# Optimization experiments

Measured on AMD Instinct MI355X. Metric: run time of the kernel, lower is better.

Reference implementation:

```python
import jax, jax.numpy as jnp
import numpy as np

KH = KW = 3  # kernel size for both convs


def conv2d_valid(x, w, b):
    # x: [B,C,H,W], w: [O,C,KH,KW], VALID padding, stride 1 (matches nn.Conv2d(3,18,3))
    y = jax.lax.conv_general_dilated(x, w, window_strides=(1, 1), padding='VALID',
                                     dimension_numbers=('NCHW', 'OIHW', 'NCHW'))
    return y + b[None, :, None, None]


def deform_conv2d(x, offset, w, b):
    # Faithful torchvision deform_conv2d: stride 1, pad 0, dilation 1, 1 group, 1 offset group.
    B, C, H, W = x.shape
    O = w.shape[0]
    Ho, Wo = offset.shape[2], offset.shape[3]
    K = KH * KW
    # offset layout: [B, 2*K, Ho, Wo], per-tap (dy, dx) interleaved, taps row-major
    off = offset.reshape(B, K, 2, Ho, Wo)
    dy, dx = off[:, :, 0], off[:, :, 1]                      # [B,K,Ho,Wo]
    ky = jnp.repeat(jnp.arange(KH), KW).astype(x.dtype)       # [K] tap row
    kx = jnp.tile(jnp.arange(KW), KH).astype(x.dtype)         # [K] tap col
    py = dy + jnp.arange(Ho, dtype=x.dtype)[None, None, :, None] + ky[None, :, None, None]
    px = dx + jnp.arange(Wo, dtype=x.dtype)[None, None, None, :] + kx[None, :, None, None]

    y0 = jnp.floor(py); x0 = jnp.floor(px)
    wy = py - y0; wx = px - x0                                # bilinear fractions
    y0i = y0.astype(jnp.int32); x0i = x0.astype(jnp.int32)

    x_flat = x.reshape(B, C, H * W)

    def corner(yi, xi):
        valid = ((yi >= 0) & (yi < H) & (xi >= 0) & (xi < W)).astype(x.dtype)  # zero pad outside
        idx = jnp.clip(yi, 0, H - 1) * W + jnp.clip(xi, 0, W - 1)              # [B,K,Ho,Wo]
        g = jax.vmap(lambda xf, ix: xf[:, ix])(x_flat, idx)                    # [B,C,K,Ho,Wo]
        return g * valid[:, None]

    val = (corner(y0i, x0i)         * ((1 - wy) * (1 - wx))[:, None]
         + corner(y0i, x0i + 1)     * ((1 - wy) * wx)[:, None]
         + corner(y0i + 1, x0i)     * (wy * (1 - wx))[:, None]
         + corner(y0i + 1, x0i + 1) * (wy * wx)[:, None])     # [B,C,K,Ho,Wo]

    out = jnp.einsum('bckhw,ock->bohw', val, w.reshape(O, C, K))
    return out + b[None, :, None, None]


def setup_inputs() -> dict:
    key = jax.random.key(0)
    k1, k2, k3, k4, k5 = jax.random.split(key, 5)
    B, C, H, W = 16, 3, 384, 384
    x = jax.random.normal(k1, (B, C, H, W), dtype=jnp.float32)
    # offset conv: Conv2d(3, 18, 3); scale down so learned offsets stay moderate
    conv_w = jax.random.normal(k2, (18, 3, KH, KW), dtype=jnp.float32) * 0.05
    conv_b = jax.random.normal(k3, (18,), dtype=jnp.float32) * 0.05
    # deform conv: DeformConv2d(3, 3, 3)
    dcn_w = jax.random.normal(k4, (3, 3, KH, KW), dtype=jnp.float32) * (1.0 / np.sqrt(3 * KH * KW))
    dcn_b = jax.random.normal(k5, (3,), dtype=jnp.float32) * 0.05
    return {'x': x, 'conv_w': conv_w, 'conv_b': conv_b, 'dcn_w': dcn_w, 'dcn_b': dcn_b}


def reference(x, conv_w, conv_b, dcn_w, dcn_b):
    offset = conv2d_valid(x, conv_w, conv_b)   # [B,18,H-2,W-2]
    return deform_conv2d(x, offset, dcn_w, dcn_b)  # [B,3,H-2,W-2]
```

## Files before the change

### kernel.cpp

```cpp
#include <hip/hip_runtime.h>

#define BATCH 16
#define CIN   3
#define H     384
#define W     384
#define HW    (H * W)
#define HO    382
#define WO    382
#define OFFC  18
#define OOUT  3
#define KTAPS 9

struct F3 { float a, b, c; };

__global__ __launch_bounds__(256)
void chw_to_hwc_kernel(const float* __restrict__ x, float* __restrict__ xt)
{
    const int gid = blockIdx.x * 256 + threadIdx.x;
    if (gid >= BATCH * HW) return;
    const int b = gid / HW;
    const int p = gid - b * HW;
    const float* xb = x + (size_t)b * (CIN * HW);
    F3 v;
    v.a = xb[p];
    v.b = xb[HW + p];
    v.c = xb[2 * HW + p];
    *(F3*)(xt + (size_t)gid * 3) = v;
}

__global__ __launch_bounds__(256)
void deform_hwc_kernel(const float* __restrict__ xt,
                       const float* __restrict__ conv_w,
                       const float* __restrict__ conv_b,
                       const float* __restrict__ dcn_w,
                       const float* __restrict__ dcn_b,
                       float* __restrict__ out)
{
    const int total = BATCH * HO * WO;
    const int gid = blockIdx.x * 256 + threadIdx.x;
    if (gid >= total) return;

    const int wo  = gid % WO;
    const int tmp = gid / WO;
    const int ho  = tmp % HO;
    const int b   = tmp / HO;

    const float* xtb = xt + (size_t)b * (HW * 3);

    F3 xp[3][3];
    #pragma unroll
    for (int i = 0; i < 3; ++i)
        #pragma unroll
        for (int j = 0; j < 3; ++j)
            xp[i][j] = *(const F3*)(xtb + (size_t)((ho + i) * W + (wo + j)) * 3);

    float off[OFFC];
    #pragma unroll
    for (int o = 0; o < OFFC; ++o) {
        float a = conv_b[o];
        #pragma unroll
        for (int i = 0; i < 3; ++i)
            #pragma unroll
            for (int j = 0; j < 3; ++j) {
                a = fmaf(conv_w[o * 27 + 0 * 9 + i * 3 + j], xp[i][j].a, a);
                a = fmaf(conv_w[o * 27 + 1 * 9 + i * 3 + j], xp[i][j].b, a);
                a = fmaf(conv_w[o * 27 + 2 * 9 + i * 3 + j], xp[i][j].c, a);
            }
        off[o] = a;
    }

    float acc0 = dcn_b[0];
    float acc1 = dcn_b[1];
    float acc2 = dcn_b[2];

    #pragma unroll
    for (int k = 0; k < KTAPS; ++k) {
        const int ky = k / 3;
        const int kx = k % 3;
        const float py = off[2 * k]     + (float)(ho + ky);
        const float px = off[2 * k + 1] + (float)(wo + kx);
        const float y0f = floorf(py);
        const float x0f = floorf(px);
        const float wy = py - y0f;
        const float wx = px - x0f;
        const int y0 = (int)y0f;
        const int x0 = (int)x0f;
        const int y1 = y0 + 1;
        const int x1 = x0 + 1;

        const bool vy0 = (unsigned)y0 < (unsigned)H;
        const bool vy1 = (unsigned)y1 < (unsigned)H;
        const bool vx0 = (unsigned)x0 < (unsigned)W;
        const bool vx1 = (unsigned)x1 < (unsigned)W;

        const int cy0 = min(max(y0, 0), H - 1);
        const int cy1 = min(max(y1, 0), H - 1);
        const int cx0 = min(max(x0, 0), W - 1);
        const int cx1 = min(max(x1, 0), W - 1);

        const float w00 = (vy0 && vx0) ? (1.f - wy) * (1.f - wx) : 0.f;
        const float w01 = (vy0 && vx1) ? (1.f - wy) * wx         : 0.f;
        const float w10 = (vy1 && vx0) ? wy * (1.f - wx)         : 0.f;
        const float w11 = (vy1 && vx1) ? wy * wx                 : 0.f;

        const F3 v00 = *(const F3*)(xtb + (size_t)(cy0 * W + cx0) * 3);
        const F3 v01 = *(const F3*)(xtb + (size_t)(cy0 * W + cx1) * 3);
        const F3 v10 = *(const F3*)(xtb + (size_t)(cy1 * W + cx0) * 3);
        const F3 v11 = *(const F3*)(xtb + (size_t)(cy1 * W + cx1) * 3);

        float s0 = v00.a * w00; s0 = fmaf(v01.a, w01, s0); s0 = fmaf(v10.a, w10, s0); s0 = fmaf(v11.a, w11, s0);
        float s1 = v00.b * w00; s1 = fmaf(v01.b, w01, s1); s1 = fmaf(v10.b, w10, s1); s1 = fmaf(v11.b, w11, s1);
        float s2 = v00.c * w00; s2 = fmaf(v01.c, w01, s2); s2 = fmaf(v10.c, w10, s2); s2 = fmaf(v11.c, w11, s2);

        acc0 = fmaf(dcn_w[0 * 27 + 0 * 9 + k], s0, acc0);
        acc0 = fmaf(dcn_w[0 * 27 + 1 * 9 + k], s1, acc0);
        acc0 = fmaf(dcn_w[0 * 27 + 2 * 9 + k], s2, acc0);
        acc1 = fmaf(dcn_w[1 * 27 + 0 * 9 + k], s0, acc1);
        acc1 = fmaf(dcn_w[1 * 27 + 1 * 9 + k], s1, acc1);
        acc1 = fmaf(dcn_w[1 * 27 + 2 * 9 + k], s2, acc1);
        acc2 = fmaf(dcn_w[2 * 27 + 0 * 9 + k], s0, acc2);
        acc2 = fmaf(dcn_w[2 * 27 + 1 * 9 + k], s1, acc2);
        acc2 = fmaf(dcn_w[2 * 27 + 2 * 9 + k], s2, acc2);
    }

    const int obase = b * (OOUT * HO * WO) + ho * WO + wo;
    __builtin_nontemporal_store(acc0, out + obase);
    __builtin_nontemporal_store(acc1, out + obase + HO * WO);
    __builtin_nontemporal_store(acc2, out + obase + 2 * HO * WO);
}

__global__ __launch_bounds__(256)
void deform_fused_kernel(const float* __restrict__ x,
                         const float* __restrict__ conv_w,
                         const float* __restrict__ conv_b,
                         const float* __restrict__ dcn_w,
                         const float* __restrict__ dcn_b,
                         float* __restrict__ out)
{
    __shared__ float s_cw[OFFC * 27];
    __shared__ float s_cb[OFFC];
    __shared__ float s_dw[OOUT * 27];
    __shared__ float s_db[OOUT];

    const int t = threadIdx.x;
    for (int i = t; i < OFFC * 27; i += 256) s_cw[i] = conv_w[i];
    if (t < OFFC)      s_cb[t] = conv_b[t];
    if (t < OOUT * 27) s_dw[t] = dcn_w[t];
    if (t < OOUT)      s_db[t] = dcn_b[t];
    __syncthreads();

    const int total = BATCH * HO * WO;
    const int gid = blockIdx.x * 256 + t;
    if (gid >= total) return;

    const int wo  = gid % WO;
    const int tmp = gid / WO;
    const int ho  = tmp % HO;
    const int b   = tmp / HO;

    const float* xb = x + b * (CIN * HW);

    float xp[CIN][3][3];
    #pragma unroll
    for (int c = 0; c < CIN; ++c) {
        const float* xc = xb + c * HW + ho * W + wo;
        #pragma unroll
        for (int i = 0; i < 3; ++i)
            #pragma unroll
            for (int j = 0; j < 3; ++j)
                xp[c][i][j] = xc[i * W + j];
    }

    float off[OFFC];
    #pragma unroll
    for (int o = 0; o < OFFC; ++o) {
        float a = s_cb[o];
        const float* wv = &s_cw[o * 27];
        #pragma unroll
        for (int c = 0; c < CIN; ++c)
            #pragma unroll
            for (int i = 0; i < 3; ++i)
                #pragma unroll
                for (int j = 0; j < 3; ++j)
                    a = fmaf(wv[c * 9 + i * 3 + j], xp[c][i][j], a);
        off[o] = a;
    }

    float a0 = s_db[0], a1 = s_db[1], a2 = s_db[2];

    #pragma unroll
    for (int k = 0; k < KTAPS; ++k) {
        const int ky = k / 3;
        const int kx = k % 3;
        const float py = off[2 * k]     + (float)(ho + ky);
        const float px = off[2 * k + 1] + (float)(wo + kx);
        const float y0f = floorf(py);
        const float x0f = floorf(px);
        const float wy = py - y0f;
        const float wx = px - x0f;
        const int y0 = (int)y0f;
        const int x0 = (int)x0f;
        const int y1 = y0 + 1;
        const int x1 = x0 + 1;
        const bool vy0 = (unsigned)y0 < (unsigned)H;
        const bool vy1 = (unsigned)y1 < (unsigned)H;
        const bool vx0 = (unsigned)x0 < (unsigned)W;
        const bool vx1 = (unsigned)x1 < (unsigned)W;
        const int cy0 = min(max(y0, 0), H - 1);
        const int cy1 = min(max(y1, 0), H - 1);
        const int cx0 = min(max(x0, 0), W - 1);
        const int cx1 = min(max(x1, 0), W - 1);
        const float w00 = (vy0 && vx0) ? (1.f - wy) * (1.f - wx) : 0.f;
        const float w01 = (vy0 && vx1) ? (1.f - wy) * wx         : 0.f;
        const float w10 = (vy1 && vx0) ? wy * (1.f - wx)         : 0.f;
        const float w11 = (vy1 && vx1) ? wy * wx                 : 0.f;
        const int i00 = cy0 * W + cx0;
        const int i01 = cy0 * W + cx1;
        const int i10 = cy1 * W + cx0;
        const int i11 = cy1 * W + cx1;
        #pragma unroll
        for (int c = 0; c < CIN; ++c) {
            const float* xc = xb + c * HW;
            float s = xc[i00] * w00;
            s = fmaf(xc[i01], w01, s);
            s = fmaf(xc[i10], w10, s);
            s = fmaf(xc[i11], w11, s);
            a0 = fmaf(s_dw[0 * 27 + c * 9 + k], s, a0);
            a1 = fmaf(s_dw[1 * 27 + c * 9 + k], s, a1);
            a2 = fmaf(s_dw[2 * 27 + c * 9 + k], s, a2);
        }
    }

    const int obase = b * (OOUT * HO * WO) + ho * WO + wo;
    __builtin_nontemporal_store(a0, out + obase);
    __builtin_nontemporal_store(a1, out + obase + HO * WO);
    __builtin_nontemporal_store(a2, out + obase + 2 * HO * WO);
}

extern "C" void kernel_launch(void* const* d_in, const int* in_sizes, int n_in,
                              void* d_out, int out_size, void* d_ws, size_t ws_size,
                              hipStream_t stream) {
    const float* x      = (const float*)d_in[0];
    const float* conv_w = (const float*)d_in[1];
    const float* conv_b = (const float*)d_in[2];
    const float* dcn_w  = (const float*)d_in[3];
    const float* dcn_b  = (const float*)d_in[4];
    float* out = (float*)d_out;

    const int total = BATCH * HO * WO;
    const size_t need = (size_t)BATCH * HW * 3 * sizeof(float);

    if (ws_size >= need) {
        float* xt = (float*)d_ws;
        chw_to_hwc_kernel<<<(BATCH * HW + 255) / 256, 256, 0, stream>>>(x, xt);
        deform_hwc_kernel<<<(total + 255) / 256, 256, 0, stream>>>(
            xt, conv_w, conv_b, dcn_w, dcn_b, out);
    } else {
        deform_fused_kernel<<<(total + 255) / 256, 256, 0, stream>>>(
            x, conv_w, conv_b, dcn_w, dcn_b, out);
    }
}
```

Measured before the change: 161.1 us.

## Use zero-padded float4 HWC staging to drop bounds checks in deform gather

Input staging now writes a float4-per-pixel HWC copy with a two-pixel zero border, so each bilinear corner fetch is one aligned 16-byte load instead of a 12-byte struct load. The new deform kernel clamps into the padded image and no longer computes per-corner validity masks, relying on the zero border for out-of-range samples. This costs a larger staging buffer and more write traffic. Offsets that push a sample more than two pixels outside the image would clamp to a border pixel instead of reading zero. The older path is kept as a fallback when the workspace is too small.

After: 156.1 us. 1.03x faster.

```diff
diff --git a/kernel.cpp b/kernel.cpp
--- a/kernel.cpp
+++ b/kernel.cpp
@@ -11,7 +11,131 @@
 #define OOUT  3
 #define KTAPS 9
 
+#define PAD   2
+#define HP    (H + 2 * PAD)
+#define WP    (W + 2 * PAD)
+
 struct F3 { float a, b, c; };
+
+__global__ __launch_bounds__(256)
+void chw_to_hwc4_kernel(const float* __restrict__ x, float4* __restrict__ xt)
+{
+    const int gid = blockIdx.x * 256 + threadIdx.x;
+    if (gid >= BATCH * HP * WP) return;
+    const int b  = gid / (HP * WP);
+    const int r2 = gid - b * (HP * WP);
+    const int ry = r2 / WP;
+    const int rx = r2 - ry * WP;
+    const int yi = ry - PAD;
+    const int xi = rx - PAD;
+    float4 v = make_float4(0.f, 0.f, 0.f, 0.f);
+    if ((unsigned)yi < (unsigned)H && (unsigned)xi < (unsigned)W) {
+        const float* xb = x + (size_t)b * (CIN * HW);
+        const int p = yi * W + xi;
+        v.x = xb[p];
+        v.y = xb[HW + p];
+        v.z = xb[2 * HW + p];
+    }
+    xt[gid] = v;
+}
+
+__global__ __launch_bounds__(256)
+void deform_pad4_kernel(const float4* __restrict__ xt,
+                        const float* __restrict__ conv_w,
+                        const float* __restrict__ conv_b,
+                        const float* __restrict__ dcn_w,
+                        const float* __restrict__ dcn_b,
+                        float* __restrict__ out)
+{
+    const int total = BATCH * HO * WO;
+    const int gid = blockIdx.x * 256 + threadIdx.x;
+    if (gid >= total) return;
+
+    const int wo  = gid % WO;
+    const int tmp = gid / WO;
+    const int ho  = tmp % HO;
+    const int b   = tmp / HO;
+
+    const float4* xtb = xt + (size_t)b * (HP * WP);
+
+    float4 xp[3][3];
+    #pragma unroll
+    for (int i = 0; i < 3; ++i) {
+        const float4* row = xtb + (ho + i + PAD) * WP + (wo + PAD);
+        xp[i][0] = row[0];
+        xp[i][1] = row[1];
+        xp[i][2] = row[2];
+    }
+
+    float off[OFFC];
+    #pragma unroll
+    for (int o = 0; o < OFFC; ++o) {
+        float a = conv_b[o];
+        #pragma unroll
+        for (int i = 0; i < 3; ++i)
+            #pragma unroll
+            for (int j = 0; j < 3; ++j) {
+                a = fmaf(conv_w[o * 27 + 0 * 9 + i * 3 + j], xp[i][j].x, a);
+                a = fmaf(conv_w[o * 27 + 1 * 9 + i * 3 + j], xp[i][j].y, a);
+                a = fmaf(conv_w[o * 27 + 2 * 9 + i * 3 + j], xp[i][j].z, a);
+            }
+        off[o] = a;
+    }
+
+    float acc0 = dcn_b[0];
+    float acc1 = dcn_b[1];
+    float acc2 = dcn_b[2];
+
+    #pragma unroll
+    for (int k = 0; k < KTAPS; ++k) {
+        const int ky = k / 3;
+        const int kx = k % 3;
+        const float oy = off[2 * k];
+        const float ox = off[2 * k + 1];
+        const float fy = floorf(oy);
+        const float fx = floorf(ox);
+        const float wy = oy - fy;
+        const float wx = ox - fx;
+
+        int iy = (int)fy + (ho + ky + PAD);
+        int ix = (int)fx + (wo + kx + PAD);
+        iy = min(max(iy, 0), HP - 2);
+        ix = min(max(ix, 0), WP - 2);
+
+        const float4* r0 = xtb + iy * WP + ix;
+        const float4* r1 = r0 + WP;
+        const float4 v00 = r0[0];
+        const float4 v01 = r0[1];
+        const float4 v10 = r1[0];
+        const float4 v11 = r1[1];
+
+        const float cwy = 1.f - wy;
+        const float cwx = 1.f - wx;
+        const float w00 = cwy * cwx;
+        const float w01 = cwy * wx;
+        const float w10 = wy * cwx;
+        const float w11 = wy * wx;
+
+        float s0 = v00.x * w00; s0 = fmaf(v01.x, w01, s0); s0 = fmaf(v10.x, w10, s0); s0 = fmaf(v11.x, w11, s0);
+        float s1 = v00.y * w00; s1 = fmaf(v01.y, w01, s1); s1 = fmaf(v10.y, w10, s1); s1 = fmaf(v11.y, w11, s1);
+        float s2 = v00.z * w00; s2 = fmaf(v01.z, w01, s2); s2 = fmaf(v10.z, w10, s2); s2 = fmaf(v11.z, w11, s2);
+
+        acc0 = fmaf(dcn_w[0 * 27 + 0 * 9 + k], s0, acc0);
+        acc0 = fmaf(dcn_w[0 * 27 + 1 * 9 + k], s1, acc0);
+        acc0 = fmaf(dcn_w[0 * 27 + 2 * 9 + k], s2, acc0);
+        acc1 = fmaf(dcn_w[1 * 27 + 0 * 9 + k], s0, acc1);
+        acc1 = fmaf(dcn_w[1 * 27 + 1 * 9 + k], s1, acc1);
+        acc1 = fmaf(dcn_w[1 * 27 + 2 * 9 + k], s2, acc1);
+        acc2 = fmaf(dcn_w[2 * 27 + 0 * 9 + k], s0, acc2);
+        acc2 = fmaf(dcn_w[2 * 27 + 1 * 9 + k], s1, acc2);
+        acc2 = fmaf(dcn_w[2 * 27 + 2 * 9 + k], s2, acc2);
+    }
+
+    const int obase = b * (OOUT * HO * WO) + ho * WO + wo;
+    __builtin_nontemporal_store(acc0, out + obase);
+    __builtin_nontemporal_store(acc1, out + obase + HO * WO);
+    __builtin_nontemporal_store(acc2, out + obase + 2 * HO * WO);
+}
 
 __global__ __launch_bounds__(256)
 void chw_to_hwc_kernel(const float* __restrict__ x, float* __restrict__ xt)
@@ -87,17 +211,14 @@
         const int x0 = (int)x0f;
         const int y1 = y0 + 1;
         const int x1 = x0 + 1;
-
         const bool vy0 = (unsigned)y0 < (unsigned)H;
         const bool vy1 = (unsigned)y1 < (unsigned)H;
         const bool vx0 = (unsigned)x0 < (unsigned)W;
         const bool vx1 = (unsigned)x1 < (unsigned)W;
-
         const int cy0 = min(max(y0, 0), H - 1);
         const int cy1 = min(max(y1, 0), H - 1);
         const int cx0 = min(max(x0, 0), W - 1);
         const int cx1 = min(max(x1, 0), W - 1);
-
         const float w00 = (vy0 && vx0) ? (1.f - wy) * (1.f - wx) : 0.f;
         const float w01 = (vy0 && vx1) ? (1.f - wy) * wx         : 0.f;
         const float w10 = (vy1 && vx0) ? wy * (1.f - wx)         : 0.f;
@@ -248,9 +369,16 @@
     float* out = (float*)d_out;
 
     const int total = BATCH * HO * WO;
-    const size_t need = (size_t)BATCH * HW * 3 * sizeof(float);
-
-    if (ws_size >= need) {
+    const size_t need4 = (size_t)BATCH * HP * WP * sizeof(float4);
+    const size_t need3 = (size_t)BATCH * HW * 3 * sizeof(float);
+
+    if (ws_size >= need4) {
+        float4* xt = (float4*)d_ws;
+        const int cells = BATCH * HP * WP;
+        chw_to_hwc4_kernel<<<(cells + 255) / 256, 256, 0, stream>>>(x, xt);
+        deform_pad4_kernel<<<(total + 255) / 256, 256, 0, stream>>>(
+            xt, conv_w, conv_b, dcn_w, dcn_b, out);
+    } else if (ws_size >= need3) {
         float* xt = (float*)d_ws;
         chw_to_hwc_kernel<<<(BATCH * HW + 255) / 256, 256, 0, stream>>>(x, xt);
         deform_hwc_kernel<<<(total + 255) / 256, 256, 0, stream>>>(
```
